# Performance work log

Hardware: AMD Instinct MI355X
Metric: run time of the kernel (lower is better)

The kernel has to match this reference:

```python
import jax, jax.numpy as jnp
import numpy as np

B, N, E, D, OUT, L = 4, 10000, 160000, 128, 64, 4
NEG = 0.01  # LeakyReLU slope

def lrelu(x):
    return jnp.where(x > 0, x, NEG * x)

def setup_inputs() -> dict:
    key = jax.random.key(0)
    ks = jax.random.split(key, 20)
    s = 0.05
    inp = {
        "x": jax.random.normal(ks[0], (B, N * 3), dtype=jnp.float32),
        "edge_index": jax.random.randint(ks[1], (2, E), 0, N, dtype=jnp.int32),
        # f0: Linear(3, D)
        "w0": jax.random.normal(ks[2], (3, D), dtype=jnp.float32) * s,
        "b0": jax.random.normal(ks[3], (D,), dtype=jnp.float32) * s,
        # per-layer params stacked on leading L axis
        "ew1": jax.random.normal(ks[4], (L, 2 * D + 1, D), dtype=jnp.float32) * s,
        "eb1": jax.random.normal(ks[5], (L, D), dtype=jnp.float32) * s,
        "ew2": jax.random.normal(ks[6], (L, D, D), dtype=jnp.float32) * s,
        "eb2": jax.random.normal(ks[7], (L, D), dtype=jnp.float32) * s,
        "cw": jax.random.normal(ks[8], (L, D, 1), dtype=jnp.float32) * s,
        "cb": jax.random.normal(ks[9], (L, 1), dtype=jnp.float32) * s,
        "nw1": jax.random.normal(ks[10], (L, 2 * D, D), dtype=jnp.float32) * s,
        "nb1": jax.random.normal(ks[11], (L, D), dtype=jnp.float32) * s,
        "nw2": jax.random.normal(ks[12], (L, D, D), dtype=jnp.float32) * s,
        "nb2": jax.random.normal(ks[13], (L, D), dtype=jnp.float32) * s,
        # project: Linear(D, OUT)
        "wp": jax.random.normal(ks[14], (D, OUT), dtype=jnp.float32) * s,
        "bp": jax.random.normal(ks[15], (OUT,), dtype=jnp.float32) * s,
    }
    return inp

def reference(x, edge_index, w0, b0, ew1, eb1, ew2, eb2, cw, cb, nw1, nb1, nw2, nb2, wp, bp):
    b = x.shape[0]
    n = x.shape[1] // 3
    pos = x.reshape(b, n, 3)            # coordinates [B,N,3]
    h = lrelu(pos @ w0 + b0)            # node features [B,N,D]
    row, col = edge_index[0], edge_index[1]
    # per-node in-edge counts (same for all layers/batches); scatter_mean -> 0 for empty nodes
    cnt = jnp.zeros((n,), x.dtype).at[col].add(1.0)
    denom = jnp.maximum(cnt, 1.0)[None, :, None]
    for i in range(L):
        rel = pos[:, row] - pos[:, col]                          # [B,E,3]
        dist_sq = jnp.sum(rel * rel, axis=-1, keepdims=True)     # [B,E,1]
        edge_in = jnp.concatenate([h[:, row], h[:, col], dist_sq], axis=-1)  # [B,E,2D+1]
        msg = lrelu(lrelu(edge_in @ ew1[i] + eb1[i]) @ ew2[i] + eb2[i])       # [B,E,D]
        aggr = jnp.zeros((b, n, msg.shape[-1]), msg.dtype).at[:, col].add(msg) / denom  # scatter_mean
        coord_update = jnp.tanh(aggr @ cw[i] + cb[i])            # [B,N,1]
        pos = pos + coord_update * 0.1
        node_in = jnp.concatenate([h, aggr], axis=-1)            # [B,N,2D]
        h = h + lrelu(lrelu(node_in @ nw1[i] + nb1[i]) @ nw2[i] + nb2[i])
    return lrelu(h.mean(axis=1) @ wp + bp)                       # [B,OUT]
```

## Files before the change

kernel.cpp:

```cpp
#include <hip/hip_runtime.h>
#include <hip/hip_bf16.h>
#include <math.h>

#define BB   4
#define NN   10000
#define NP   10112
#define EE   160000
#define DD   128
#define OUTD 64
#define LL   4
#define NEGS 0.01f
#define MSTR 136
#define RSF  68

typedef __attribute__((ext_vector_type(8))) short   short8;
typedef __attribute__((ext_vector_type(4))) float   floatx4;
typedef __attribute__((ext_vector_type(4))) uint    uintx4;

__device__ __forceinline__ float lrelu(float x) { return fmaxf(x, NEGS * x); }
__device__ __forceinline__ ushort f2bf(float x) {
    uint u = __builtin_bit_cast(uint, x);
    return (ushort)((u + 0x7FFFu + ((u >> 16) & 1u)) >> 16);
}
__device__ __forceinline__ float bf2f(ushort u) {
    uint v = ((uint)u) << 16;
    return __builtin_bit_cast(float, v);
}
__device__ __forceinline__ float bcf(uint u) { return __builtin_bit_cast(float, u); }

__global__ void k_cvtw_all(const float* __restrict__ ew1, const float* __restrict__ ew2,
                           const float* __restrict__ nw1, const float* __restrict__ nw2,
                           ushort* __restrict__ wtopf, ushort* __restrict__ wmidf,
                           ushort* __restrict__ ew2f, ushort* __restrict__ nw1f,
                           ushort* __restrict__ nw2f) {
    int tid = blockIdx.x * 256 + threadIdx.x;
    const float* src; ushort* dst; int pitch, nks, loc;
    if (tid < 8192)       { src = ew1;                     dst = wtopf; pitch = 257; nks = 4; loc = tid; }
    else if (tid < 16384) { src = ew1 + (size_t)128 * DD;  dst = wmidf; pitch = 257; nks = 4; loc = tid - 8192; }
    else if (tid < 24576) { src = ew2;                     dst = ew2f;  pitch = 128; nks = 4; loc = tid - 16384; }
    else if (tid < 40960) { src = nw1;                     dst = nw1f;  pitch = 256; nks = 8; loc = tid - 24576; }
    else                  { src = nw2;                     dst = nw2f;  pitch = 128; nks = 4; loc = tid - 40960; }
    int lane = loc & 63;
    int nt   = (loc >> 6) & 7;
    int ks   = (loc >> 9) % nks;
    int l    = loc / (nks * 512);
    int quad = lane >> 4, l16 = lane & 15;
    int n = nt * 16 + l16;
    const float* s = src + (size_t)l * pitch * DD;
    ushort* d = dst + (size_t)loc * 8;
    #pragma unroll
    for (int j = 0; j < 8; ++j)
        d[j] = f2bf(s[(size_t)(ks * 32 + quad * 8 + j) * DD + n]);
}

__global__ void k_h0(const float* __restrict__ x, const float* __restrict__ w0,
                     const float* __restrict__ b0, ushort* __restrict__ hb) {
    int idx = blockIdx.x * 256 + threadIdx.x;
    if (idx >= BB * NP * DD) return;
    int d  = idx & (DD - 1);
    int bn = idx >> 7;
    int n  = bn % NP, b = bn / NP;
    float v = 0.0f;
    if (n < NN) {
        const float* p = x + ((size_t)b * NN + n) * 3;
        v = lrelu(b0[d] + p[0] * w0[d] + p[1] * w0[DD + d] + p[2] * w0[2 * DD + d]);
    }
    hb[idx] = f2bf(v);
}

__global__ void k_count(const int* __restrict__ col, float* __restrict__ cnt,
                        int* __restrict__ ecnt) {
    int e = blockIdx.x * blockDim.x + threadIdx.x;
    if (e < EE) {
        int c = col[e];
        atomicAdd(&cnt[c], 1.0f);
        atomicAdd(&ecnt[c], 1);
    }
}

__global__ __launch_bounds__(256) void k_scan(const int* __restrict__ ecnt,
                                              int* __restrict__ cursor) {
    __shared__ int s_sum[256];
    int t = threadIdx.x;
    int base = t * 40;
    int s = 0;
    for (int i = 0; i < 40; ++i) {
        int n = base + i;
        if (n < NN) s += ecnt[n];
    }
    s_sum[t] = s;
    __syncthreads();
    if (t == 0) {
        int a = 0;
        for (int i = 0; i < 256; ++i) { int v = s_sum[i]; s_sum[i] = a; a += v; }
    }
    __syncthreads();
    int a = s_sum[t];
    for (int i = 0; i < 40; ++i) {
        int n = base + i;
        if (n < NN) { cursor[n] = a; a += ecnt[n]; }
    }
}

__global__ void k_place(const int* __restrict__ row, const int* __restrict__ col,
                        int* __restrict__ cursor,
                        int* __restrict__ rowS, int* __restrict__ colS) {
    int e = blockIdx.x * blockDim.x + threadIdx.x;
    if (e >= EE) return;
    int c = col[e];
    int p = atomicAdd(&cursor[c], 1);
    rowS[p] = row[e];
    colS[p] = c;
}

__global__ __launch_bounds__(256) void k_pq(
    const ushort* __restrict__ hb, const ushort* __restrict__ wtf,
    const ushort* __restrict__ wmf, const float* __restrict__ b1,
    ushort* __restrict__ P, ushort* __restrict__ Q)
{
    __shared__ __align__(16) ushort s_out[64 * MSTR];
    const int g = blockIdx.x;
    const int b = (g >> 1) & 3;
    const int n0 = ((g >> 3) * 2 + (g & 1)) * 64;
    const int t = threadIdx.x;
    const int w = t >> 6, lane = t & 63, quad = lane >> 4, l16 = lane & 15;
    const int rw = w * 16;
    const int nw = n0 + rw;

    const ushort* hptr = hb + ((size_t)b * NP + nw + l16) * DD;
    float b1r[8];
    #pragma unroll
    for (int nt = 0; nt < 8; ++nt) b1r[nt] = b1[nt * 16 + l16];

    const short8* wt = (const short8*)wtf;
    const short8* wm = (const short8*)wmf;

    #pragma unroll
    for (int pass = 0; pass < 2; ++pass) {
        floatx4 ap[8];
        #pragma unroll
        for (int nt = 0; nt < 8; ++nt)
            #pragma unroll
            for (int r = 0; r < 4; ++r) ap[nt][r] = pass ? b1r[nt] : 0.0f;
        const short8* wv = pass ? wm : wt;
        #pragma unroll
        for (int ks = 0; ks < 4; ++ks) {
            short8 bf[8];
            #pragma unroll
            for (int nt = 0; nt < 8; ++nt) bf[nt] = wv[(ks * 8 + nt) * 64 + lane];
            short8 af = *(const short8*)(hptr + ks * 32 + quad * 8);
            #pragma unroll
            for (int nt = 0; nt < 8; ++nt)
                ap[nt] = __builtin_amdgcn_mfma_f32_16x16x32_bf16(af, bf[nt], ap[nt], 0, 0, 0);
        }
        #pragma unroll
        for (int nt = 0; nt < 8; ++nt)
            #pragma unroll
            for (int r = 0; r < 4; ++r)
                s_out[(rw + quad * 4 + r) * MSTR + nt * 16 + l16] = f2bf(ap[nt][r]);
        ushort* dst = pass ? Q : P;
        #pragma unroll
        for (int i = 0; i < 4; ++i) {
            int row = rw + i * 4 + quad;
            short8 v = *(const short8*)&s_out[row * MSTR + l16 * 8];
            *(short8*)(dst + ((size_t)b * NP + n0 + row) * DD + l16 * 8) = v;
        }
    }
}

__global__ __launch_bounds__(256, 4) void k_edge(
    const float* __restrict__ pos,
    const ushort* __restrict__ P, const ushort* __restrict__ Q,
    const int* __restrict__ rowS, const int* __restrict__ colS,
    const float* __restrict__ w1last,
    const ushort* __restrict__ w2f, const float* __restrict__ b2,
    float* __restrict__ aggr)
{
    __shared__ int    s_row[128];
    __shared__ int    s_col[128];
    __shared__ float  s_ds[128];
    __shared__ float  s_red[128 * RSF];

    const int g    = blockIdx.x;
    const int b    = (g >> 1) & 3;
    const int tile = (g >> 3) * 2 + (g & 1);
    const int e0   = tile * 128;
    const int t    = threadIdx.x;
    const int w    = t >> 6, lane = t & 63;
    const int quad = lane >> 4, l16 = lane & 15;

    if (t < 128) {
        int e = e0 + t;
        int r = rowS[e], c = colS[e];
        s_row[t] = r;
        s_col[t] = c;
        const float* pr = pos + ((size_t)b * NN + r) * 3;
        const float* pc = pos + ((size_t)b * NN + c) * 3;
        float dx = pr[0] - pc[0], dy = pr[1] - pc[1], dz = pr[2] - pc[2];
        s_ds[t] = dx * dx + dy * dy + dz * dz;
    }
    __syncthreads();

    const int ew = w * 32;
    const ushort* pp[2];
    const ushort* qp[2];
    float dsv[2];
    #pragma unroll
    for (int mt = 0; mt < 2; ++mt) {
        int el = ew + mt * 16 + l16;
        pp[mt]  = P + ((size_t)b * NP + s_row[el]) * DD;
        qp[mt]  = Q + ((size_t)b * NP + s_col[el]) * DD;
        dsv[mt] = s_ds[el];
    }

    uintx4 pf[2][4], qf[2][4];
    #pragma unroll
    for (int ks = 0; ks < 4; ++ks) {
        const int koff = ks * 32 + quad * 8;
        #pragma unroll
        for (int mt = 0; mt < 2; ++mt) {
            pf[mt][ks] = *(const uintx4*)(pp[mt] + koff);
            qf[mt][ks] = *(const uintx4*)(qp[mt] + koff);
        }
    }

    uintx4 mid[2][4];
    #pragma unroll
    for (int ks = 0; ks < 4; ++ks) {
        const int koff = ks * 32 + quad * 8;
        floatx4 wl0 = *(const floatx4*)(w1last + koff);
        floatx4 wl1 = *(const floatx4*)(w1last + koff + 4);
        float wl[8] = {wl0[0], wl0[1], wl0[2], wl0[3], wl1[0], wl1[1], wl1[2], wl1[3]};
        #pragma unroll
        for (int mt = 0; mt < 2; ++mt) {
            #pragma unroll
            for (int i = 0; i < 4; ++i) {
                uint pv = pf[mt][ks][i], qv = qf[mt][ks][i];
                float vlo = lrelu(bcf(pv << 16) + bcf(qv << 16) + dsv[mt] * wl[2 * i]);
                float vhi = lrelu(bcf(pv & 0xFFFF0000u) + bcf(qv & 0xFFFF0000u) + dsv[mt] * wl[2 * i + 1]);
                mid[mt][ks][i] = (__builtin_bit_cast(uint, vlo) >> 16) |
                                 (__builtin_bit_cast(uint, vhi) & 0xFFFF0000u);
            }
        }
    }

    float b2r[8];
    #pragma unroll
    for (int nt = 0; nt < 8; ++nt) b2r[nt] = b2[nt * 16 + l16];

    const short8* w2v = (const short8*)w2f;
    #pragma unroll
    for (int ph = 0; ph < 2; ++ph) {
        floatx4 acc[2][4];
        #pragma unroll
        for (int mt = 0; mt < 2; ++mt)
            #pragma unroll
            for (int ntl = 0; ntl < 4; ++ntl)
                #pragma unroll
                for (int r = 0; r < 4; ++r) acc[mt][ntl][r] = b2r[ph * 4 + ntl];

        #pragma unroll
        for (int ks = 0; ks < 4; ++ks) {
            short8 bf[4];
            #pragma unroll
            for (int ntl = 0; ntl < 4; ++ntl)
                bf[ntl] = w2v[(ks * 8 + ph * 4 + ntl) * 64 + lane];
            #pragma unroll
            for (int mt = 0; mt < 2; ++mt) {
                short8 af = __builtin_bit_cast(short8, mid[mt][ks]);
                #pragma unroll
                for (int ntl = 0; ntl < 4; ++ntl)
                    acc[mt][ntl] = __builtin_amdgcn_mfma_f32_16x16x32_bf16(af, bf[ntl], acc[mt][ntl], 0, 0, 0);
            }
        }

        #pragma unroll
        for (int mt = 0; mt < 2; ++mt)
            #pragma unroll
            for (int ntl = 0; ntl < 4; ++ntl)
                #pragma unroll
                for (int r = 0; r < 4; ++r)
                    s_red[(ew + mt * 16 + quad * 4 + r) * RSF + ntl * 16 + l16] =
                        lrelu(acc[mt][ntl][r]);

        const int d = ph * 64 + lane;
        float run = 0.0f;
        int prev = s_col[ew];
        for (int r = 0; r < 32; ++r) {
            int cid = s_col[ew + r];
            float v = s_red[(ew + r) * RSF + lane];
            if (cid != prev) {
                atomicAdd(&aggr[((size_t)b * NP + prev) * DD + d], run);
                run = 0.0f;
                prev = cid;
            }
            run += v;
        }
        atomicAdd(&aggr[((size_t)b * NP + prev) * DD + d], run);
    }
}

__global__ __launch_bounds__(256) void k_node(
    ushort* hb, float* aggr, const float* __restrict__ cnt,
    const float* __restrict__ cw, const float* __restrict__ cb,
    const ushort* __restrict__ w1f, const float* __restrict__ b1,
    const ushort* __restrict__ w2f, const float* __restrict__ b2,
    float* __restrict__ pos,
    int do_pq,
    const ushort* __restrict__ wtn, const ushort* __restrict__ wmn,
    const float* __restrict__ b1n,
    ushort* __restrict__ P, ushort* __restrict__ Q)
{
    __shared__ __align__(16) ushort s_mid[64 * MSTR];
    __shared__ __align__(16) ushort s_ho[64 * MSTR];

    const int g    = blockIdx.x;
    const int b    = (g >> 1) & 3;
    const int n0   = ((g >> 3) * 2 + (g & 1)) * 64;
    const int t    = threadIdx.x;
    const int w    = t >> 6, lane = t & 63;
    const int quad = lane >> 4, l16 = lane & 15;
    const int rw   = w * 16;
    const int nw   = n0 + rw;

    #pragma unroll
    for (int i = 0; i < 4; ++i) {
        int row = rw + i * 4 + quad;
        short8 v = *(const short8*)(hb + ((size_t)b * NP + n0 + row) * DD + l16 * 8);
        *(short8*)&s_ho[row * MSTR + l16 * 8] = v;
    }

    float* aptr = aggr + ((size_t)b * NP + nw + l16) * DD;
    float inv = 0.0f;
    {
        int node = nw + l16;
        if (node < NN) { float dn = cnt[node]; inv = 1.0f / fmaxf(dn, 1.0f); }
    }
    float b1r[8], b2r[8];
    #pragma unroll
    for (int nt = 0; nt < 8; ++nt) {
        int d = nt * 16 + l16;
        b1r[nt] = b1[d]; b2r[nt] = b2[d];
    }

    floatx4 acc[8];
    #pragma unroll
    for (int nt = 0; nt < 8; ++nt)
        #pragma unroll
        for (int r = 0; r < 4; ++r) acc[nt][r] = b1r[nt];

    float cwacc = 0.0f;
    const floatx4 zero4 = {0.0f, 0.0f, 0.0f, 0.0f};
    const short8* w1v = (const short8*)w1f;
    #pragma unroll
    for (int ks = 0; ks < 8; ++ks) {
        short8 bf[8];
        #pragma unroll
        for (int nt = 0; nt < 8; ++nt) bf[nt] = w1v[(ks * 8 + nt) * 64 + lane];
        const int koff = (ks & 3) * 32 + quad * 8;
        if (ks < 4) {
            short8 af = *(const short8*)(&s_ho[(rw + l16) * MSTR + koff]);
            #pragma unroll
            for (int nt = 0; nt < 8; ++nt)
                acc[nt] = __builtin_amdgcn_mfma_f32_16x16x32_bf16(af, bf[nt], acc[nt], 0, 0, 0);
        } else {
            floatx4 cw0 = *(const floatx4*)(cw + koff);
            floatx4 cw1 = *(const floatx4*)(cw + koff + 4);
            floatx4 a0 = *(const floatx4*)(aptr + koff);
            floatx4 a1 = *(const floatx4*)(aptr + koff + 4);
            *(floatx4*)(aptr + koff)     = zero4;
            *(floatx4*)(aptr + koff + 4) = zero4;
            short8 af;
            #pragma unroll
            for (int j = 0; j < 4; ++j) {
                float v = a0[j] * inv;
                af[j] = (short)f2bf(v);
                cwacc += v * cw0[j];
            }
            #pragma unroll
            for (int j = 0; j < 4; ++j) {
                float v = a1[j] * inv;
                af[4 + j] = (short)f2bf(v);
                cwacc += v * cw1[j];
            }
            #pragma unroll
            for (int nt = 0; nt < 8; ++nt)
                acc[nt] = __builtin_amdgcn_mfma_f32_16x16x32_bf16(af, bf[nt], acc[nt], 0, 0, 0);
        }
    }

    {
        float full = cwacc;
        full += __shfl_xor(full, 16);
        full += __shfl_xor(full, 32);
        int node = nw + l16;
        if (quad == 0 && node < NN) {
            float cu = 0.1f * tanhf(full + cb[0]);
            float* pp = pos + ((size_t)b * NN + node) * 3;
            pp[0] += cu; pp[1] += cu; pp[2] += cu;
        }
    }

    #pragma unroll
    for (int nt = 0; nt < 8; ++nt)
        #pragma unroll
        for (int r = 0; r < 4; ++r)
            s_mid[(rw + quad * 4 + r) * MSTR + nt * 16 + l16] = f2bf(lrelu(acc[nt][r]));

    floatx4 acc2[8];
    #pragma unroll
    for (int nt = 0; nt < 8; ++nt)
        #pragma unroll
        for (int r = 0; r < 4; ++r) acc2[nt][r] = b2r[nt];

    const short8* w2v = (const short8*)w2f;
    #pragma unroll
    for (int ks = 0; ks < 4; ++ks) {
        short8 bf[8];
        #pragma unroll
        for (int nt = 0; nt < 8; ++nt) bf[nt] = w2v[(ks * 8 + nt) * 64 + lane];
        short8 af = *(const short8*)(&s_mid[(rw + l16) * MSTR + ks * 32 + quad * 8]);
        #pragma unroll
        for (int nt = 0; nt < 8; ++nt)
            acc2[nt] = __builtin_amdgcn_mfma_f32_16x16x32_bf16(af, bf[nt], acc2[nt], 0, 0, 0);
    }

    #pragma unroll
    for (int nt = 0; nt < 8; ++nt)
        #pragma unroll
        for (int r = 0; r < 4; ++r) {
            int row = rw + quad * 4 + r;
            float hold = bf2f(s_ho[row * MSTR + nt * 16 + l16]);
            float hv = hold + lrelu(acc2[nt][r]);
            s_mid[row * MSTR + nt * 16 + l16] = f2bf(hv);
        }

    #pragma unroll
    for (int i = 0; i < 4; ++i) {
        int row = rw + i * 4 + quad;
        int n = n0 + row;
        short8 v = *(const short8*)&s_mid[row * MSTR + l16 * 8];
        if (n < NN)
            *(short8*)(hb + ((size_t)b * NP + n) * DD + l16 * 8) = v;
    }

    if (do_pq) {
        const short8* wt = (const short8*)wtn;
        const short8* wm = (const short8*)wmn;
        float b1nr[8];
        #pragma unroll
        for (int nt = 0; nt < 8; ++nt) b1nr[nt] = b1n[nt * 16 + l16];

        #pragma unroll
        for (int pass = 0; pass < 2; ++pass) {
            floatx4 ap[8];
            #pragma unroll
            for (int nt = 0; nt < 8; ++nt)
                #pragma unroll
                for (int r = 0; r < 4; ++r) ap[nt][r] = pass ? b1nr[nt] : 0.0f;
            const short8* wv = pass ? wm : wt;
            #pragma unroll
            for (int ks = 0; ks < 4; ++ks) {
                short8 bf[8];
                #pragma unroll
                for (int nt = 0; nt < 8; ++nt) bf[nt] = wv[(ks * 8 + nt) * 64 + lane];
                short8 af = *(const short8*)(&s_mid[(rw + l16) * MSTR + ks * 32 + quad * 8]);
                #pragma unroll
                for (int nt = 0; nt < 8; ++nt)
                    ap[nt] = __builtin_amdgcn_mfma_f32_16x16x32_bf16(af, bf[nt], ap[nt], 0, 0, 0);
            }
            #pragma unroll
            for (int nt = 0; nt < 8; ++nt)
                #pragma unroll
                for (int r = 0; r < 4; ++r)
                    s_ho[(rw + quad * 4 + r) * MSTR + nt * 16 + l16] = f2bf(ap[nt][r]);
            ushort* dst = pass ? Q : P;
            #pragma unroll
            for (int i = 0; i < 4; ++i) {
                int row = rw + i * 4 + quad;
                short8 v = *(const short8*)&s_ho[row * MSTR + l16 * 8];
                *(short8*)(dst + ((size_t)b * NP + n0 + row) * DD + l16 * 8) = v;
            }
        }
    }
}

#define NPC 50
__global__ void k_mean(const ushort* __restrict__ hb, float* __restrict__ hm) {
    int b  = blockIdx.y;
    int n0 = blockIdx.x * NPC;
    int d  = threadIdx.x;
    float s = 0.0f;
    for (int n = n0; n < n0 + NPC; ++n) s += bf2f(hb[((size_t)b * NP + n) * DD + d]);
    atomicAdd(&hm[b * DD + d], s);
}

__global__ void k_proj(const float* __restrict__ hm, const float* __restrict__ wp,
                       const float* __restrict__ bp, float* __restrict__ out) {
    int t = threadIdx.x;
    int b = t >> 6, o = t & (OUTD - 1);
    float s = 0.0f;
    for (int d2 = 0; d2 < DD; ++d2) s += hm[b * DD + d2] * wp[d2 * OUTD + o];
    s = s * (1.0f / NN) + bp[o];
    out[b * OUTD + o] = lrelu(s);
}

extern "C" void kernel_launch(void* const* d_in, const int* in_sizes, int n_in,
                              void* d_out, int out_size, void* d_ws, size_t ws_size,
                              hipStream_t stream) {
    (void)in_sizes; (void)n_in; (void)out_size; (void)ws_size;
    const float* x   = (const float*)d_in[0];
    const int*   ei  = (const int*)d_in[1];
    const float* w0  = (const float*)d_in[2];
    const float* b0  = (const float*)d_in[3];
    const float* ew1 = (const float*)d_in[4];
    const float* eb1 = (const float*)d_in[5];
    const float* ew2 = (const float*)d_in[6];
    const float* eb2 = (const float*)d_in[7];
    const float* cw  = (const float*)d_in[8];
    const float* cb  = (const float*)d_in[9];
    const float* nw1 = (const float*)d_in[10];
    const float* nb1 = (const float*)d_in[11];
    const float* nw2 = (const float*)d_in[12];
    const float* nb2 = (const float*)d_in[13];
    const float* wp  = (const float*)d_in[14];
    const float* bp  = (const float*)d_in[15];
    const int* row = ei;
    const int* col = ei + EE;

    const size_t HSZ = (size_t)BB * NP * DD;
    float* ws   = (float*)d_ws;
    float* aggr = ws;
    float* pos  = aggr + HSZ;
    float* cnt  = pos + (size_t)BB * NN * 3;
    float* hm   = cnt + NN;
    ushort* hb    = (ushort*)(hm + 512);
    ushort* Pb    = hb + HSZ;
    ushort* Qb    = Pb + HSZ;
    ushort* wtopf = Qb + HSZ;
    ushort* wmidf = wtopf + (size_t)LL * 16384;
    ushort* ew2f  = wmidf + (size_t)LL * 16384;
    ushort* nw1f  = ew2f + (size_t)LL * 16384;
    ushort* nw2f  = nw1f + (size_t)LL * 32768;
    int* ecnt   = (int*)(nw2f + (size_t)LL * 16384);
    int* cursor = ecnt + NN;
    int* rowS   = cursor + NN;
    int* colS   = rowS + EE;

    hipMemcpyAsync(pos, x, sizeof(float) * (size_t)BB * NN * 3,
                   hipMemcpyDeviceToDevice, stream);
    hipMemsetAsync(cnt, 0, sizeof(float) * NN, stream);
    hipMemsetAsync(ecnt, 0, sizeof(int) * NN, stream);
    hipMemsetAsync(hm, 0, sizeof(float) * BB * DD, stream);
    hipMemsetAsync(aggr, 0, sizeof(float) * HSZ, stream);

    k_cvtw_all<<<192, 256, 0, stream>>>(ew1, ew2, nw1, nw2,
                                        wtopf, wmidf, ew2f, nw1f, nw2f);

    k_h0<<<((int)HSZ + 255) / 256, 256, 0, stream>>>(x, w0, b0, hb);
    k_count<<<(EE + 255) / 256, 256, 0, stream>>>(col, cnt, ecnt);
    k_scan<<<1, 256, 0, stream>>>(ecnt, cursor);
    k_place<<<(EE + 255) / 256, 256, 0, stream>>>(row, col, cursor, rowS, colS);

    k_pq<<<(NP / 64) * BB, 256, 0, stream>>>(hb, wtopf, wmidf, eb1, Pb, Qb);

    for (int i = 0; i < LL; ++i) {
        k_edge<<<(EE / 128) * BB, 256, 0, stream>>>(
            pos, Pb, Qb, rowS, colS,
            ew1 + (size_t)i * 257 * DD + (size_t)256 * DD,
            ew2f + (size_t)i * 16384,
            eb2 + (size_t)i * DD,
            aggr);
        int nx = (i < LL - 1) ? (i + 1) : i;
        k_node<<<(NP / 64) * BB, 256, 0, stream>>>(
            hb, aggr, cnt,
            cw + (size_t)i * DD, cb + i,
            nw1f + (size_t)i * 32768, nb1 + (size_t)i * DD,
            nw2f + (size_t)i * 16384, nb2 + (size_t)i * DD,
            pos,
            (i < LL - 1) ? 1 : 0,
            wtopf + (size_t)nx * 16384, wmidf + (size_t)nx * 16384,
            eb1 + (size_t)nx * DD,
            Pb, Qb);
    }

    k_mean<<<dim3(NN / NPC, BB), DD, 0, stream>>>(hb, hm);
    k_proj<<<1, 256, 0, stream>>>(hm, wp, bp, (float*)d_out);
}
```

Measured before the change: 593.6 us.

## Partition edge kernel by destination node tiles with shared-memory aggregation

The edge kernel now assigns each block a tile of 32 destination nodes and loops over that tile's CSR edge range, using the cursor array, in chunks of 128 edges. Partial sums are accumulated with shared-memory atomics and the tile is written to global aggr directly. This removes global atomics, the aggr memset and the re-zeroing stores in the node kernel. The per-edge message staging buffer also moves to bf16 to save LDS. The cost is load imbalance between tiles with different in-degree, partially filled final chunks, extra bf16 rounding before the sum, and higher LDS use that may lower occupancy.

Result: slower. 1.909 ms (+221.6%).

```diff
diff --git a/kernel.cpp b/kernel.cpp
--- a/kernel.cpp
+++ b/kernel.cpp
@@ -11,7 +11,8 @@
 #define LL   4
 #define NEGS 0.01f
 #define MSTR 136
-#define RSF  68
+#define RSH  68
+#define NTB  32
 
 typedef __attribute__((ext_vector_type(8))) short   short8;
 typedef __attribute__((ext_vector_type(4))) float   floatx4;
@@ -172,136 +173,168 @@
     const float* __restrict__ pos,
     const ushort* __restrict__ P, const ushort* __restrict__ Q,
     const int* __restrict__ rowS, const int* __restrict__ colS,
+    const int* __restrict__ cursor,
     const float* __restrict__ w1last,
     const ushort* __restrict__ w2f, const float* __restrict__ b2,
     float* __restrict__ aggr)
 {
     __shared__ int    s_row[128];
-    __shared__ int    s_col[128];
+    __shared__ int    s_colL[128];
     __shared__ float  s_ds[128];
-    __shared__ float  s_red[128 * RSF];
+    __shared__ __align__(16) ushort s_red[128 * RSH];
+    __shared__ __align__(16) float  s_aggr[NTB * DD];
 
     const int g    = blockIdx.x;
     const int b    = (g >> 1) & 3;
-    const int tile = (g >> 3) * 2 + (g & 1);
-    const int e0   = tile * 128;
+    const int n0   = ((g >> 3) * 2 + (g & 1)) * NTB;
     const int t    = threadIdx.x;
     const int w    = t >> 6, lane = t & 63;
     const int quad = lane >> 4, l16 = lane & 15;
-
-    if (t < 128) {
-        int e = e0 + t;
-        int r = rowS[e], c = colS[e];
-        s_row[t] = r;
-        s_col[t] = c;
-        const float* pr = pos + ((size_t)b * NN + r) * 3;
-        const float* pc = pos + ((size_t)b * NN + c) * 3;
-        float dx = pr[0] - pc[0], dy = pr[1] - pc[1], dz = pr[2] - pc[2];
-        s_ds[t] = dx * dx + dy * dy + dz * dz;
-    }
+    const int ew   = w * 32;
+
+    const int e_start = (n0 == 0) ? 0 : cursor[((n0 <= NN) ? n0 : NN) - 1];
+    const int e_end   = cursor[(n0 + NTB - 1 < NN) ? (n0 + NTB - 1) : (NN - 1)];
+    const int ec      = e_end - e_start;
+    const int nch     = (ec + 127) >> 7;
+
+    {
+        floatx4* za = (floatx4*)s_aggr;
+        #pragma unroll
+        for (int i = 0; i < 4; ++i) za[t + i * 256] = (floatx4){0.f, 0.f, 0.f, 0.f};
+    }
+
+    float b2r[8];
+    #pragma unroll
+    for (int nt = 0; nt < 8; ++nt) b2r[nt] = b2[nt * 16 + l16];
+    const short8* w2v = (const short8*)w2f;
+
+    for (int c = 0; c < nch; ++c) {
+        __syncthreads();
+        if (t < 128) {
+            int be = c * 128 + t;
+            int r = 0, cl = 0; float dsq = 0.0f;
+            if (be < ec) {
+                int e = e_start + be;
+                r = rowS[e];
+                int cc = colS[e];
+                cl = cc - n0;
+                const float* pr = pos + ((size_t)b * NN + r) * 3;
+                const float* pc = pos + ((size_t)b * NN + cc) * 3;
+                float dx = pr[0] - pc[0], dy = pr[1] - pc[1], dz = pr[2] - pc[2];
+                dsq = dx * dx + dy * dy + dz * dz;
+            }
+            s_row[t] = r;
+            s_colL[t] = cl;
+            s_ds[t] = dsq;
+        }
+        __syncthreads();
+
+        const ushort* pp[2];
+        const ushort* qp[2];
+        float dsv[2];
+        #pragma unroll
+        for (int mt = 0; mt < 2; ++mt) {
+            int el = ew + mt * 16 + l16;
+            pp[mt]  = P + ((size_t)b * NP + s_row[el]) * DD;
+            qp[mt]  = Q + ((size_t)b * NP + n0 + s_colL[el]) * DD;
+            dsv[mt] = s_ds[el];
+        }
+
+        uintx4 pf[2][4], qf[2][4];
+        #pragma unroll
+        for (int ks = 0; ks < 4; ++ks) {
+            const int koff = ks * 32 + quad * 8;
+            #pragma unroll
+            for (int mt = 0; mt < 2; ++mt) {
+                pf[mt][ks] = *(const uintx4*)(pp[mt] + koff);
+                qf[mt][ks] = *(const uintx4*)(qp[mt] + koff);
+            }
+        }
+
+        uintx4 mid[2][4];
+        #pragma unroll
+        for (int ks = 0; ks < 4; ++ks) {
+            const int koff = ks * 32 + quad * 8;
+            floatx4 wl0 = *(const floatx4*)(w1last + koff);
+            floatx4 wl1 = *(const floatx4*)(w1last + koff + 4);
+            float wl[8] = {wl0[0], wl0[1], wl0[2], wl0[3], wl1[0], wl1[1], wl1[2], wl1[3]};
+            #pragma unroll
+            for (int mt = 0; mt < 2; ++mt) {
+                #pragma unroll
+                for (int i = 0; i < 4; ++i) {
+                    uint pv = pf[mt][ks][i], qv = qf[mt][ks][i];
+                    float vlo = lrelu(bcf(pv << 16) + bcf(qv << 16) + dsv[mt] * wl[2 * i]);
+                    float vhi = lrelu(bcf(pv & 0xFFFF0000u) + bcf(qv & 0xFFFF0000u) + dsv[mt] * wl[2 * i + 1]);
+                    mid[mt][ks][i] = (__builtin_bit_cast(uint, vlo) >> 16) |
+                                     (__builtin_bit_cast(uint, vhi) & 0xFFFF0000u);
+                }
+            }
+        }
+
+        const int lim = ec - c * 128 - ew;
+        #pragma unroll
+        for (int ph = 0; ph < 2; ++ph) {
+            floatx4 acc[2][4];
+            #pragma unroll
+            for (int mt = 0; mt < 2; ++mt)
+                #pragma unroll
+                for (int ntl = 0; ntl < 4; ++ntl)
+                    #pragma unroll
+                    for (int r = 0; r < 4; ++r) acc[mt][ntl][r] = b2r[ph * 4 + ntl];
+
+            #pragma unroll
+            for (int ks = 0; ks < 4; ++ks) {
+                short8 bf[4];
+                #pragma unroll
+                for (int ntl = 0; ntl < 4; ++ntl)
+                    bf[ntl] = w2v[(ks * 8 + ph * 4 + ntl) * 64 + lane];
+                #pragma unroll
+                for (int mt = 0; mt < 2; ++mt) {
+                    short8 af = __builtin_bit_cast(short8, mid[mt][ks]);
+                    #pragma unroll
+                    for (int ntl = 0; ntl < 4; ++ntl)
+                        acc[mt][ntl] = __builtin_amdgcn_mfma_f32_16x16x32_bf16(af, bf[ntl], acc[mt][ntl], 0, 0, 0);
+                }
+            }
+
+            #pragma unroll
+            for (int mt = 0; mt < 2; ++mt)
+                #pragma unroll
+                for (int ntl = 0; ntl < 4; ++ntl)
+                    #pragma unroll
+                    for (int r = 0; r < 4; ++r)
+                        s_red[(ew + mt * 16 + quad * 4 + r) * RSH + ntl * 16 + l16] =
+                            f2bf(lrelu(acc[mt][ntl][r]));
+
+            const int d = ph * 64 + lane;
+            float run = 0.0f;
+            int prev = s_colL[ew];
+            for (int r = 0; r < 32; ++r) {
+                int cid = s_colL[ew + r];
+                float v = (r < lim) ? bf2f(s_red[(ew + r) * RSH + lane]) : 0.0f;
+                if (cid != prev) {
+                    atomicAdd(&s_aggr[prev * DD + d], run);
+                    run = 0.0f;
+                    prev = cid;
+                }
+                run += v;
+            }
+            atomicAdd(&s_aggr[prev * DD + d], run);
+        }
+    }
+
     __syncthreads();
-
-    const int ew = w * 32;
-    const ushort* pp[2];
-    const ushort* qp[2];
-    float dsv[2];
-    #pragma unroll
-    for (int mt = 0; mt < 2; ++mt) {
-        int el = ew + mt * 16 + l16;
-        pp[mt]  = P + ((size_t)b * NP + s_row[el]) * DD;
-        qp[mt]  = Q + ((size_t)b * NP + s_col[el]) * DD;
-        dsv[mt] = s_ds[el];
-    }
-
-    uintx4 pf[2][4], qf[2][4];
-    #pragma unroll
-    for (int ks = 0; ks < 4; ++ks) {
-        const int koff = ks * 32 + quad * 8;
-        #pragma unroll
-        for (int mt = 0; mt < 2; ++mt) {
-            pf[mt][ks] = *(const uintx4*)(pp[mt] + koff);
-            qf[mt][ks] = *(const uintx4*)(qp[mt] + koff);
-        }
-    }
-
-    uintx4 mid[2][4];
-    #pragma unroll
-    for (int ks = 0; ks < 4; ++ks) {
-        const int koff = ks * 32 + quad * 8;
-        floatx4 wl0 = *(const floatx4*)(w1last + koff);
-        floatx4 wl1 = *(const floatx4*)(w1last + koff + 4);
-        float wl[8] = {wl0[0], wl0[1], wl0[2], wl0[3], wl1[0], wl1[1], wl1[2], wl1[3]};
-        #pragma unroll
-        for (int mt = 0; mt < 2; ++mt) {
-            #pragma unroll
-            for (int i = 0; i < 4; ++i) {
-                uint pv = pf[mt][ks][i], qv = qf[mt][ks][i];
-                float vlo = lrelu(bcf(pv << 16) + bcf(qv << 16) + dsv[mt] * wl[2 * i]);
-                float vhi = lrelu(bcf(pv & 0xFFFF0000u) + bcf(qv & 0xFFFF0000u) + dsv[mt] * wl[2 * i + 1]);
-                mid[mt][ks][i] = (__builtin_bit_cast(uint, vlo) >> 16) |
-                                 (__builtin_bit_cast(uint, vhi) & 0xFFFF0000u);
-            }
-        }
-    }
-
-    float b2r[8];
-    #pragma unroll
-    for (int nt = 0; nt < 8; ++nt) b2r[nt] = b2[nt * 16 + l16];
-
-    const short8* w2v = (const short8*)w2f;
-    #pragma unroll
-    for (int ph = 0; ph < 2; ++ph) {
-        floatx4 acc[2][4];
-        #pragma unroll
-        for (int mt = 0; mt < 2; ++mt)
-            #pragma unroll
-            for (int ntl = 0; ntl < 4; ++ntl)
-                #pragma unroll
-                for (int r = 0; r < 4; ++r) acc[mt][ntl][r] = b2r[ph * 4 + ntl];
-
-        #pragma unroll
-        for (int ks = 0; ks < 4; ++ks) {
-            short8 bf[4];
-            #pragma unroll
-            for (int ntl = 0; ntl < 4; ++ntl)
-                bf[ntl] = w2v[(ks * 8 + ph * 4 + ntl) * 64 + lane];
-            #pragma unroll
-            for (int mt = 0; mt < 2; ++mt) {
-                short8 af = __builtin_bit_cast(short8, mid[mt][ks]);
-                #pragma unroll
-                for (int ntl = 0; ntl < 4; ++ntl)
-                    acc[mt][ntl] = __builtin_amdgcn_mfma_f32_16x16x32_bf16(af, bf[ntl], acc[mt][ntl], 0, 0, 0);
-            }
-        }
-
-        #pragma unroll
-        for (int mt = 0; mt < 2; ++mt)
-            #pragma unroll
-            for (int ntl = 0; ntl < 4; ++ntl)
-                #pragma unroll
-                for (int r = 0; r < 4; ++r)
-                    s_red[(ew + mt * 16 + quad * 4 + r) * RSF + ntl * 16 + l16] =
-                        lrelu(acc[mt][ntl][r]);
-
-        const int d = ph * 64 + lane;
-        float run = 0.0f;
-        int prev = s_col[ew];
-        for (int r = 0; r < 32; ++r) {
-            int cid = s_col[ew + r];
-            float v = s_red[(ew + r) * RSF + lane];
-            if (cid != prev) {
-                atomicAdd(&aggr[((size_t)b * NP + prev) * DD + d], run);
-                run = 0.0f;
-                prev = cid;
-            }
-            run += v;
-        }
-        atomicAdd(&aggr[((size_t)b * NP + prev) * DD + d], run);
+    {
+        float* dst = aggr + ((size_t)b * NP + n0) * DD;
+        const floatx4* sa = (const floatx4*)s_aggr;
+        floatx4* da = (floatx4*)dst;
+        #pragma unroll
+        for (int i = 0; i < 4; ++i) da[t + i * 256] = sa[t + i * 256];
     }
 }
 
 __global__ __launch_bounds__(256) void k_node(
-    ushort* hb, float* aggr, const float* __restrict__ cnt,
+    ushort* hb, const float* __restrict__ aggr, const float* __restrict__ cnt,
     const float* __restrict__ cw, const float* __restrict__ cb,
     const ushort* __restrict__ w1f, const float* __restrict__ b1,
     const ushort* __restrict__ w2f, const float* __restrict__ b2,
@@ -330,7 +363,7 @@
         *(short8*)&s_ho[row * MSTR + l16 * 8] = v;
     }
 
-    float* aptr = aggr + ((size_t)b * NP + nw + l16) * DD;
+    const float* aptr = aggr + ((size_t)b * NP + nw + l16) * DD;
     float inv = 0.0f;
     {
         int node = nw + l16;
@@ -350,7 +383,6 @@
         for (int r = 0; r < 4; ++r) acc[nt][r] = b1r[nt];
 
     float cwacc = 0.0f;
-    const floatx4 zero4 = {0.0f, 0.0f, 0.0f, 0.0f};
     const short8* w1v = (const short8*)w1f;
     #pragma unroll
     for (int ks = 0; ks < 8; ++ks) {
@@ -368,8 +400,6 @@
             floatx4 cw1 = *(const floatx4*)(cw + koff + 4);
             floatx4 a0 = *(const floatx4*)(aptr + koff);
             floatx4 a1 = *(const floatx4*)(aptr + koff + 4);
-            *(floatx4*)(aptr + koff)     = zero4;
-            *(floatx4*)(aptr + koff + 4) = zero4;
             short8 af;
             #pragma unroll
             for (int j = 0; j < 4; ++j) {
@@ -552,7 +582,6 @@
     hipMemsetAsync(cnt, 0, sizeof(float) * NN, stream);
     hipMemsetAsync(ecnt, 0, sizeof(int) * NN, stream);
     hipMemsetAsync(hm, 0, sizeof(float) * BB * DD, stream);
-    hipMemsetAsync(aggr, 0, sizeof(float) * HSZ, stream);
 
     k_cvtw_all<<<192, 256, 0, stream>>>(ew1, ew2, nw1, nw2,
                                         wtopf, wmidf, ew2f, nw1f, nw2f);
@@ -565,8 +594,8 @@
     k_pq<<<(NP / 64) * BB, 256, 0, stream>>>(hb, wtopf, wmidf, eb1, Pb, Qb);
 
     for (int i = 0; i < LL; ++i) {
-        k_edge<<<(EE / 128) * BB, 256, 0, stream>>>(
-            pos, Pb, Qb, rowS, colS,
+        k_edge<<<(NP / NTB) * BB, 256, 0, stream>>>(
+            pos, Pb, Qb, rowS, colS, cursor,
             ew1 + (size_t)i * 257 * DD + (size_t)256 * DD,
             ew2f + (size_t)i * 16384,
             eb2 + (size_t)i * DD,
```

## Halve node-kernel tile to 32 rows and split output columns across wave pairs

Applied to the files above, without the earlier changes.

The node-update kernel now processes 32 nodes per block instead of 64. Pairs of waves share a 16-row group and each computes half of the 128 output columns, with block barriers for shared staging. Clearing of the aggregation buffer becomes a block-wide coalesced store after the reads complete. This doubles the grid and halves per-wave accumulator registers to improve occupancy, at the cost of extra barriers and more total weight fetches.

Result: no change. 601.8 us (+1.4%).

```diff
diff --git a/kernel.cpp b/kernel.cpp
--- a/kernel.cpp
+++ b/kernel.cpp
@@ -311,66 +311,63 @@
     const float* __restrict__ b1n,
     ushort* __restrict__ P, ushort* __restrict__ Q)
 {
-    __shared__ __align__(16) ushort s_mid[64 * MSTR];
-    __shared__ __align__(16) ushort s_ho[64 * MSTR];
+    __shared__ __align__(16) ushort s_ho[32 * MSTR];
+    __shared__ __align__(16) ushort s_mid[32 * MSTR];
 
     const int g    = blockIdx.x;
     const int b    = (g >> 1) & 3;
-    const int n0   = ((g >> 3) * 2 + (g & 1)) * 64;
+    const int n0   = ((g >> 3) * 2 + (g & 1)) * 32;
     const int t    = threadIdx.x;
     const int w    = t >> 6, lane = t & 63;
     const int quad = lane >> 4, l16 = lane & 15;
-    const int rw   = w * 16;
-    const int nw   = n0 + rw;
-
-    #pragma unroll
-    for (int i = 0; i < 4; ++i) {
-        int row = rw + i * 4 + quad;
+    const int gi   = w >> 1;
+    const int ch   = w & 1;
+    const int rg   = gi * 16;
+
+    #pragma unroll
+    for (int i = 0; i < 2; ++i) {
+        int row = w * 8 + i * 4 + quad;
         short8 v = *(const short8*)(hb + ((size_t)b * NP + n0 + row) * DD + l16 * 8);
         *(short8*)&s_ho[row * MSTR + l16 * 8] = v;
     }
-
-    float* aptr = aggr + ((size_t)b * NP + nw + l16) * DD;
+    __syncthreads();
+
+    float* aptr = aggr + ((size_t)b * NP + n0 + rg + l16) * DD;
+    const int node = n0 + rg + l16;
     float inv = 0.0f;
-    {
-        int node = nw + l16;
-        if (node < NN) { float dn = cnt[node]; inv = 1.0f / fmaxf(dn, 1.0f); }
-    }
-    float b1r[8], b2r[8];
-    #pragma unroll
-    for (int nt = 0; nt < 8; ++nt) {
-        int d = nt * 16 + l16;
-        b1r[nt] = b1[d]; b2r[nt] = b2[d];
-    }
-
-    floatx4 acc[8];
-    #pragma unroll
-    for (int nt = 0; nt < 8; ++nt)
-        #pragma unroll
-        for (int r = 0; r < 4; ++r) acc[nt][r] = b1r[nt];
+    if (node < NN) { float dn = cnt[node]; inv = 1.0f / fmaxf(dn, 1.0f); }
+
+    float b1r[4], b2r[4];
+    #pragma unroll
+    for (int ntl = 0; ntl < 4; ++ntl) {
+        int d = (ch * 4 + ntl) * 16 + l16;
+        b1r[ntl] = b1[d]; b2r[ntl] = b2[d];
+    }
+
+    floatx4 acc[4];
+    #pragma unroll
+    for (int ntl = 0; ntl < 4; ++ntl)
+        #pragma unroll
+        for (int r = 0; r < 4; ++r) acc[ntl][r] = b1r[ntl];
 
     float cwacc = 0.0f;
     const floatx4 zero4 = {0.0f, 0.0f, 0.0f, 0.0f};
     const short8* w1v = (const short8*)w1f;
     #pragma unroll
     for (int ks = 0; ks < 8; ++ks) {
-        short8 bf[8];
-        #pragma unroll
-        for (int nt = 0; nt < 8; ++nt) bf[nt] = w1v[(ks * 8 + nt) * 64 + lane];
+        short8 bf[4];
+        #pragma unroll
+        for (int ntl = 0; ntl < 4; ++ntl)
+            bf[ntl] = w1v[(ks * 8 + ch * 4 + ntl) * 64 + lane];
         const int koff = (ks & 3) * 32 + quad * 8;
+        short8 af;
         if (ks < 4) {
-            short8 af = *(const short8*)(&s_ho[(rw + l16) * MSTR + koff]);
-            #pragma unroll
-            for (int nt = 0; nt < 8; ++nt)
-                acc[nt] = __builtin_amdgcn_mfma_f32_16x16x32_bf16(af, bf[nt], acc[nt], 0, 0, 0);
+            af = *(const short8*)(&s_ho[(rg + l16) * MSTR + koff]);
         } else {
             floatx4 cw0 = *(const floatx4*)(cw + koff);
             floatx4 cw1 = *(const floatx4*)(cw + koff + 4);
             floatx4 a0 = *(const floatx4*)(aptr + koff);
             floatx4 a1 = *(const floatx4*)(aptr + koff + 4);
-            *(floatx4*)(aptr + koff)     = zero4;
-            *(floatx4*)(aptr + koff + 4) = zero4;
-            short8 af;
             #pragma unroll
             for (int j = 0; j < 4; ++j) {
                 float v = a0[j] * inv;
@@ -383,18 +380,17 @@
                 af[4 + j] = (short)f2bf(v);
                 cwacc += v * cw1[j];
             }
-            #pragma unroll
-            for (int nt = 0; nt < 8; ++nt)
-                acc[nt] = __builtin_amdgcn_mfma_f32_16x16x32_bf16(af, bf[nt], acc[nt], 0, 0, 0);
-        }
+        }
+        #pragma unroll
+        for (int ntl = 0; ntl < 4; ++ntl)
+            acc[ntl] = __builtin_amdgcn_mfma_f32_16x16x32_bf16(af, bf[ntl], acc[ntl], 0, 0, 0);
     }
 
     {
         float full = cwacc;
         full += __shfl_xor(full, 16);
         full += __shfl_xor(full, 32);
-        int node = nw + l16;
-        if (quad == 0 && node < NN) {
+        if (ch == 0 && quad == 0 && node < NN) {
             float cu = 0.1f * tanhf(full + cb[0]);
             float* pp = pos + ((size_t)b * NN + node) * 3;
             pp[0] += cu; pp[1] += cu; pp[2] += cu;
@@ -402,44 +398,53 @@
     }
 
     #pragma unroll
-    for (int nt = 0; nt < 8; ++nt)
+    for (int ntl = 0; ntl < 4; ++ntl)
         #pragma unroll
         for (int r = 0; r < 4; ++r)
-            s_mid[(rw + quad * 4 + r) * MSTR + nt * 16 + l16] = f2bf(lrelu(acc[nt][r]));
-
-    floatx4 acc2[8];
-    #pragma unroll
-    for (int nt = 0; nt < 8; ++nt)
-        #pragma unroll
-        for (int r = 0; r < 4; ++r) acc2[nt][r] = b2r[nt];
+            s_mid[(rg + quad * 4 + r) * MSTR + (ch * 4 + ntl) * 16 + l16] =
+                f2bf(lrelu(acc[ntl][r]));
+    __syncthreads();
+
+    {
+        floatx4* za = (floatx4*)(aggr + ((size_t)b * NP + n0) * DD);
+        #pragma unroll
+        for (int i = 0; i < 4; ++i) za[t + i * 256] = zero4;
+    }
+
+    floatx4 acc2[4];
+    #pragma unroll
+    for (int ntl = 0; ntl < 4; ++ntl)
+        #pragma unroll
+        for (int r = 0; r < 4; ++r) acc2[ntl][r] = b2r[ntl];
 
     const short8* w2v = (const short8*)w2f;
     #pragma unroll
     for (int ks = 0; ks < 4; ++ks) {
-        short8 bf[8];
-        #pragma unroll
-        for (int nt = 0; nt < 8; ++nt) bf[nt] = w2v[(ks * 8 + nt) * 64 + lane];
-        short8 af = *(const short8*)(&s_mid[(rw + l16) * MSTR + ks * 32 + quad * 8]);
-        #pragma unroll
-        for (int nt = 0; nt < 8; ++nt)
-            acc2[nt] = __builtin_amdgcn_mfma_f32_16x16x32_bf16(af, bf[nt], acc2[nt], 0, 0, 0);
-    }
-
-    #pragma unroll
-    for (int nt = 0; nt < 8; ++nt)
+        short8 bf[4];
+        #pragma unroll
+        for (int ntl = 0; ntl < 4; ++ntl)
+            bf[ntl] = w2v[(ks * 8 + ch * 4 + ntl) * 64 + lane];
+        short8 af = *(const short8*)(&s_mid[(rg + l16) * MSTR + ks * 32 + quad * 8]);
+        #pragma unroll
+        for (int ntl = 0; ntl < 4; ++ntl)
+            acc2[ntl] = __builtin_amdgcn_mfma_f32_16x16x32_bf16(af, bf[ntl], acc2[ntl], 0, 0, 0);
+    }
+
+    #pragma unroll
+    for (int ntl = 0; ntl < 4; ++ntl)
         #pragma unroll
         for (int r = 0; r < 4; ++r) {
-            int row = rw + quad * 4 + r;
-            float hold = bf2f(s_ho[row * MSTR + nt * 16 + l16]);
-            float hv = hold + lrelu(acc2[nt][r]);
-            s_mid[row * MSTR + nt * 16 + l16] = f2bf(hv);
-        }
-
-    #pragma unroll
-    for (int i = 0; i < 4; ++i) {
-        int row = rw + i * 4 + quad;
+            int off = (rg + quad * 4 + r) * MSTR + (ch * 4 + ntl) * 16 + l16;
+            float hold = bf2f(s_ho[off]);
+            s_ho[off] = f2bf(hold + lrelu(acc2[ntl][r]));
+        }
+    __syncthreads();
+
+    #pragma unroll
+    for (int i = 0; i < 2; ++i) {
+        int row = w * 8 + i * 4 + quad;
         int n = n0 + row;
-        short8 v = *(const short8*)&s_mid[row * MSTR + l16 * 8];
+        short8 v = *(const short8*)&s_ho[row * MSTR + l16 * 8];
         if (n < NN)
             *(short8*)(hb + ((size_t)b * NP + n) * DD + l16 * 8) = v;
     }
@@ -447,40 +452,44 @@
     if (do_pq) {
         const short8* wt = (const short8*)wtn;
         const short8* wm = (const short8*)wmn;
-        float b1nr[8];
-        #pragma unroll
-        for (int nt = 0; nt < 8; ++nt) b1nr[nt] = b1n[nt * 16 + l16];
+        float b1nr[4];
+        #pragma unroll
+        for (int ntl = 0; ntl < 4; ++ntl) b1nr[ntl] = b1n[(ch * 4 + ntl) * 16 + l16];
 
         #pragma unroll
         for (int pass = 0; pass < 2; ++pass) {
-            floatx4 ap[8];
-            #pragma unroll
-            for (int nt = 0; nt < 8; ++nt)
-                #pragma unroll
-                for (int r = 0; r < 4; ++r) ap[nt][r] = pass ? b1nr[nt] : 0.0f;
+            floatx4 ap[4];
+            #pragma unroll
+            for (int ntl = 0; ntl < 4; ++ntl)
+                #pragma unroll
+                for (int r = 0; r < 4; ++r) ap[ntl][r] = pass ? b1nr[ntl] : 0.0f;
             const short8* wv = pass ? wm : wt;
             #pragma unroll
             for (int ks = 0; ks < 4; ++ks) {
-                short8 bf[8];
-                #pragma unroll
-                for (int nt = 0; nt < 8; ++nt) bf[nt] = wv[(ks * 8 + nt) * 64 + lane];
-                short8 af = *(const short8*)(&s_mid[(rw + l16) * MSTR + ks * 32 + quad * 8]);
-                #pragma unroll
-                for (int nt = 0; nt < 8; ++nt)
-                    ap[nt] = __builtin_amdgcn_mfma_f32_16x16x32_bf16(af, bf[nt], ap[nt], 0, 0, 0);
-            }
-            #pragma unroll
-            for (int nt = 0; nt < 8; ++nt)
+                short8 bf[4];
+                #pragma unroll
+                for (int ntl = 0; ntl < 4; ++ntl)
+                    bf[ntl] = wv[(ks * 8 + ch * 4 + ntl) * 64 + lane];
+                short8 af = *(const short8*)(&s_ho[(rg + l16) * MSTR + ks * 32 + quad * 8]);
+                #pragma unroll
+                for (int ntl = 0; ntl < 4; ++ntl)
+                    ap[ntl] = __builtin_amdgcn_mfma_f32_16x16x32_bf16(af, bf[ntl], ap[ntl], 0, 0, 0);
+            }
+            #pragma unroll
+            for (int ntl = 0; ntl < 4; ++ntl)
                 #pragma unroll
                 for (int r = 0; r < 4; ++r)
-                    s_ho[(rw + quad * 4 + r) * MSTR + nt * 16 + l16] = f2bf(ap[nt][r]);
+                    s_mid[(rg + quad * 4 + r) * MSTR + (ch * 4 + ntl) * 16 + l16] =
+                        f2bf(ap[ntl][r]);
+            __syncthreads();
             ushort* dst = pass ? Q : P;
             #pragma unroll
-            for (int i = 0; i < 4; ++i) {
-                int row = rw + i * 4 + quad;
-                short8 v = *(const short8*)&s_ho[row * MSTR + l16 * 8];
+            for (int i = 0; i < 2; ++i) {
+                int row = w * 8 + i * 4 + quad;
+                short8 v = *(const short8*)&s_mid[row * MSTR + l16 * 8];
                 *(short8*)(dst + ((size_t)b * NP + n0 + row) * DD + l16 * 8) = v;
             }
+            __syncthreads();
         }
     }
 }
@@ -572,7 +581,7 @@
             eb2 + (size_t)i * DD,
             aggr);
         int nx = (i < LL - 1) ? (i + 1) : i;
-        k_node<<<(NP / 64) * BB, 256, 0, stream>>>(
+        k_node<<<(NP / 32) * BB, 256, 0, stream>>>(
             hb, aggr, cnt,
             cw + (size_t)i * DD, cb + i,
             nw1f + (size_t)i * 32768, nb1 + (size_t)i * DD,
```
